# Performance work log

Hardware: AMD Instinct MI355X
Metric: run time of the kernel (lower is better)

## Reference

```python
import jax, jax.numpy as jnp
import numpy as np

B, H, W, P = 2, 224, 224, 256


def setup_inputs() -> dict:
    key = jax.random.key(0)
    ks = jax.random.split(key, 7)
    x = jax.random.normal(ks[0], (B, 1, H, W), dtype=jnp.float32)
    offset_x1 = jax.random.uniform(ks[1], (P,), jnp.float32, -16.0, 16.0)
    offset_x2 = jax.random.uniform(ks[2], (P,), jnp.float32, -16.0, 16.0)
    offset_y1 = jax.random.uniform(ks[3], (P,), jnp.float32, -16.0, 16.0)
    offset_y2 = jax.random.uniform(ks[4], (P,), jnp.float32, -16.0, 16.0)
    radii = jax.random.randint(ks[5], (P,), 1, 4).astype(jnp.int32)  # {1,2,3}
    thresholds = jax.random.normal(ks[6], (P,), dtype=jnp.float32) * 0.1
    return {
        'x': x,
        'offset_x1': offset_x1, 'offset_x2': offset_x2,
        'offset_y1': offset_y1, 'offset_y2': offset_y2,
        'radii': radii, 'thresholds': thresholds,
        'max_radius': 3,
    }


def reference(x, offset_x1, offset_x2, offset_y1, offset_y2, radii, thresholds, max_radius):
    Bb, _, Hh, Ww = x.shape
    r = int(max_radius)
    dtype = x.dtype
    # replicate-padded integral image, zero-padded by 1 on top/left -> [B, Hp+1, Wp+1]
    xp = jnp.pad(x, ((0, 0), (0, 0), (r, r), (r, r)), mode='edge')
    integral = jnp.cumsum(jnp.cumsum(xp, axis=2), axis=3)
    integral = jnp.pad(integral, ((0, 0), (0, 0), (1, 0), (1, 0)))[:, 0]

    base_y = jnp.arange(Hh, dtype=dtype)[None, :, None]   # [1,H,1]
    base_x = jnp.arange(Ww, dtype=dtype)[None, None, :]   # [1,1,W]
    rad = radii.astype(jnp.int32)[:, None, None]           # [P,1,1]
    area = ((2.0 * radii.astype(dtype) + 1.0) ** 2)[:, None, None]

    def box_mean(off_y, off_x):
        # clamped float centers, truncated to int (non-negative -> trunc == floor)
        cy = jnp.clip(base_y + off_y[:, None, None], 0.0, Hh - 1).astype(jnp.int32) + r
        cx = jnp.clip(base_x + off_x[:, None, None], 0.0, Ww - 1).astype(jnp.int32) + r
        y0, x0 = cy - rad, cx - rad
        y1, x1 = cy + rad + 1, cx + rad + 1
        g = lambda yi, xi: integral[:, yi, xi]  # gather -> [B,P,H,W]
        s = g(y1, x1) - g(y0, x1) - g(y1, x0) + g(y0, x0)
        return s / area

    diff = box_mean(offset_y1, offset_x1) - box_mean(offset_y2, offset_x2)
    # binarize=False: return centered differences
    return diff - thresholds[None, :, None, None].astype(diff.dtype)
```

## Files before the change

### kernel.cpp

```cpp
#include <hip/hip_runtime.h>

#define BN 2
#define HN 224
#define WN 224
#define PN 256
#define RN 3
#define IW 231
#define ISZ (IW * IW)
#define NPIX (HN * WN)

__global__ __launch_bounds__(256) void integral_rows_kernel(
    const float* __restrict__ x, float* __restrict__ I)
{
    const int wave = (blockIdx.x * 256 + threadIdx.x) >> 6;
    const int lane = threadIdx.x & 63;
    if (wave >= BN * IW) return;
    const int b = wave / IW, i = wave % IW;
    float* Ib = I + b * ISZ + i * IW;
    if (i == 0) {
        for (int j = lane; j < IW; j += 64) Ib[j] = 0.0f;
        return;
    }
    int yy = i - 1 - RN;
    yy = yy < 0 ? 0 : (yy > HN - 1 ? HN - 1 : yy);
    const float* xr = x + b * HN * WN + yy * WN;

    float carry = 0.0f;
#pragma unroll
    for (int c = 0; c < 4; ++c) {
        const int j = c * 64 + lane;
        float v = 0.0f;
        if (j >= 1 && j < IW) {
            int xx = j - 1 - RN;
            xx = xx < 0 ? 0 : (xx > WN - 1 ? WN - 1 : xx);
            v = xr[xx];
        }
#pragma unroll
        for (int d = 1; d < 64; d <<= 1) {
            float n = __shfl_up(v, d, 64);
            if (lane >= d) v += n;
        }
        v += carry;
        if (j < IW) Ib[j] = v;
        carry = __shfl(v, 63, 64);
    }
}

__global__ __launch_bounds__(256) void integral_cols_kernel(float* __restrict__ I)
{
    const int t = blockIdx.x * 256 + threadIdx.x;
    if (t >= BN * IW) return;
    const int b = t / IW, j = t % IW;
    float* Ib = I + b * ISZ;
    float acc = 0.0f;
#pragma unroll 11
    for (int i = 1; i < IW; ++i) {
        acc += Ib[i * IW + j];
        Ib[i * IW + j] = acc;
    }
}

__global__ __launch_bounds__(256) void bad_main_kernel(
    const float* __restrict__ I,
    const float* __restrict__ ox1, const float* __restrict__ ox2,
    const float* __restrict__ oy1, const float* __restrict__ oy2,
    const int*   __restrict__ radii, const float* __restrict__ thr,
    float* __restrict__ out)
{
    const int p  = blockIdx.y;
    const int b  = blockIdx.z;
    const int xt = blockIdx.x & 3;
    const int yt = blockIdx.x >> 2;
    const int x  = xt * 64 + threadIdx.x;
    const int y0 = yt * (HN / 2) + threadIdx.y;

    const float offx1 = ox1[p], offx2 = ox2[p];
    const float offy1 = oy1[p], offy2 = oy2[p];
    const int   rad   = radii[p];
    const float t     = thr[p];
    const float side  = (float)(2 * rad + 1);
    const float inv_area = 1.0f / (side * side);

    const float* Ib = I + b * ISZ;

    const float fx = (float)x;
    const int cx1 = (int)fminf(fmaxf(fx + offx1, 0.0f), (float)(WN - 1)) + RN;
    const int a0 = cx1 - rad, a1 = cx1 + rad + 1;
    const int cx2 = (int)fminf(fmaxf(fx + offx2, 0.0f), (float)(WN - 1)) + RN;
    const int b0 = cx2 - rad, b1 = cx2 + rad + 1;

    const bool xok = (x < WN);
    float* outp = out + (size_t)(b * PN + p) * NPIX + (size_t)y0 * WN;

#pragma unroll 4
    for (int i = 0; i < HN / 2; i += 4) {
        const int y = y0 + i;
        const float fy = (float)y;
        const int cy1 = __builtin_amdgcn_readfirstlane(
                            (int)fminf(fmaxf(fy + offy1, 0.0f), (float)(HN - 1))) + RN;
        const int cy2 = __builtin_amdgcn_readfirstlane(
                            (int)fminf(fmaxf(fy + offy2, 0.0f), (float)(HN - 1))) + RN;
        const float* r1lo = Ib + (cy1 - rad) * IW;
        const float* r1hi = Ib + (cy1 + rad + 1) * IW;
        const float* r2lo = Ib + (cy2 - rad) * IW;
        const float* r2hi = Ib + (cy2 + rad + 1) * IW;

        const float s1 = r1hi[a1] - r1lo[a1] - r1hi[a0] + r1lo[a0];
        const float s2 = r2hi[b1] - r2lo[b1] - r2hi[b0] + r2lo[b0];

        if (xok) outp[i * WN + x] = (s1 - s2) * inv_area - t;
    }
}

extern "C" void kernel_launch(void* const* d_in, const int* in_sizes, int n_in,
                              void* d_out, int out_size, void* d_ws, size_t ws_size,
                              hipStream_t stream)
{
    const float* x    = (const float*)d_in[0];
    const float* ox1  = (const float*)d_in[1];
    const float* ox2  = (const float*)d_in[2];
    const float* oy1  = (const float*)d_in[3];
    const float* oy2  = (const float*)d_in[4];
    const int*   rad  = (const int*)d_in[5];
    const float* thr  = (const float*)d_in[6];

    float* I   = (float*)d_ws;
    float* out = (float*)d_out;

    hipLaunchKernelGGL(integral_rows_kernel, dim3((BN * IW * 64 + 255) / 256), dim3(256), 0, stream, x, I);
    hipLaunchKernelGGL(integral_cols_kernel, dim3((BN * IW + 255) / 256), dim3(256), 0, stream, I);
    hipLaunchKernelGGL(bad_main_kernel,      dim3(8, PN, BN), dim3(64, 4, 1), 0, stream,
                       I, ox1, ox2, oy1, oy2, rad, thr, out);
}
```

Measured before the change: 161.6 us.

## Precompute per-radius box-mean maps and gather them in the main kernel

Adds a kernel that computes a box-mean map for each of the three possible radii and each batch from the integral image. The main kernel then gathers two values per output pixel from the map for that pattern's radius, instead of eight integral-image reads plus the area scaling. This cuts gather traffic in the dominant output-writing kernel, which is bound by its output stores. The cost is an extra launch and extra workspace, and it assumes radii fall in 1..3 and BN is 2 (the index uses zb&1).

```diff
diff --git a/kernel.cpp b/kernel.cpp
--- a/kernel.cpp
+++ b/kernel.cpp
@@ -60,8 +60,30 @@
     }
 }
 
+__global__ __launch_bounds__(256) void box_mean_kernel(
+    const float* __restrict__ I, float* __restrict__ BM)
+{
+    const int xt = blockIdx.x;
+    const int zb = blockIdx.z;
+    const int r_idx = zb >> 1, b = zb & 1;
+    const int rad = r_idx + 1;
+    const float inv_area = 1.0f / (float)((2 * rad + 1) * (2 * rad + 1));
+    const int x = xt * 64 + threadIdx.x;
+    const int xc = x < WN ? x : WN - 1;
+    const int y = blockIdx.y * 4 + threadIdx.y;
+
+    const float* Ib = I + b * ISZ;
+    const int y0 = y + RN - rad, y1 = y + RN + rad + 1;
+    const int x0 = xc + RN - rad, x1 = xc + RN + rad + 1;
+    const float* rlo = Ib + y0 * IW;
+    const float* rhi = Ib + y1 * IW;
+    const float s = rhi[x1] - rlo[x1] - rhi[x0] + rlo[x0];
+    if (x < WN)
+        BM[(size_t)zb * NPIX + y * WN + x] = s * inv_area;
+}
+
 __global__ __launch_bounds__(256) void bad_main_kernel(
-    const float* __restrict__ I,
+    const float* __restrict__ BM,
     const float* __restrict__ ox1, const float* __restrict__ ox2,
     const float* __restrict__ oy1, const float* __restrict__ oy2,
     const int*   __restrict__ radii, const float* __restrict__ thr,
@@ -78,37 +100,26 @@
     const float offy1 = oy1[p], offy2 = oy2[p];
     const int   rad   = radii[p];
     const float t     = thr[p];
-    const float side  = (float)(2 * rad + 1);
-    const float inv_area = 1.0f / (side * side);
 
-    const float* Ib = I + b * ISZ;
+    const float* map = BM + (size_t)((rad - 1) * BN + b) * NPIX;
 
     const float fx = (float)x;
-    const int cx1 = (int)fminf(fmaxf(fx + offx1, 0.0f), (float)(WN - 1)) + RN;
-    const int a0 = cx1 - rad, a1 = cx1 + rad + 1;
-    const int cx2 = (int)fminf(fmaxf(fx + offx2, 0.0f), (float)(WN - 1)) + RN;
-    const int b0 = cx2 - rad, b1 = cx2 + rad + 1;
+    const int vx1 = (int)fminf(fmaxf(fx + offx1, 0.0f), (float)(WN - 1));
+    const int vx2 = (int)fminf(fmaxf(fx + offx2, 0.0f), (float)(WN - 1));
 
     const bool xok = (x < WN);
     float* outp = out + (size_t)(b * PN + p) * NPIX + (size_t)y0 * WN;
 
 #pragma unroll 4
     for (int i = 0; i < HN / 2; i += 4) {
-        const int y = y0 + i;
-        const float fy = (float)y;
+        const float fy = (float)(y0 + i);
         const int cy1 = __builtin_amdgcn_readfirstlane(
-                            (int)fminf(fmaxf(fy + offy1, 0.0f), (float)(HN - 1))) + RN;
+                            (int)fminf(fmaxf(fy + offy1, 0.0f), (float)(HN - 1)));
         const int cy2 = __builtin_amdgcn_readfirstlane(
-                            (int)fminf(fmaxf(fy + offy2, 0.0f), (float)(HN - 1))) + RN;
-        const float* r1lo = Ib + (cy1 - rad) * IW;
-        const float* r1hi = Ib + (cy1 + rad + 1) * IW;
-        const float* r2lo = Ib + (cy2 - rad) * IW;
-        const float* r2hi = Ib + (cy2 + rad + 1) * IW;
-
-        const float s1 = r1hi[a1] - r1lo[a1] - r1hi[a0] + r1lo[a0];
-        const float s2 = r2hi[b1] - r2lo[b1] - r2hi[b0] + r2lo[b0];
-
-        if (xok) outp[i * WN + x] = (s1 - s2) * inv_area - t;
+                            (int)fminf(fmaxf(fy + offy2, 0.0f), (float)(HN - 1)));
+        const float v1 = map[cy1 * WN + vx1];
+        const float v2 = map[cy2 * WN + vx2];
+        if (xok) outp[i * WN + x] = v1 - v2 - t;
     }
 }
 
@@ -124,11 +135,13 @@
     const int*   rad  = (const int*)d_in[5];
     const float* thr  = (const float*)d_in[6];
 
-    float* I   = (float*)d_ws;
+    float* I  = (float*)d_ws;
+    float* BM = I + BN * ISZ;
     float* out = (float*)d_out;
 
     hipLaunchKernelGGL(integral_rows_kernel, dim3((BN * IW * 64 + 255) / 256), dim3(256), 0, stream, x, I);
     hipLaunchKernelGGL(integral_cols_kernel, dim3((BN * IW + 255) / 256), dim3(256), 0, stream, I);
+    hipLaunchKernelGGL(box_mean_kernel,      dim3(4, HN / 4, 6), dim3(64, 4, 1), 0, stream, I, BM);
     hipLaunchKernelGGL(bad_main_kernel,      dim3(8, PN, BN), dim3(64, 4, 1), 0, stream,
-                       I, ox1, ox2, oy1, oy2, rad, thr, out);
+                       BM, ox1, ox2, oy1, oy2, rad, thr, out);
 }
```

Result: faster. 148.5 us (-8.1%).
